# Optimization experiments

Measured on AMD Instinct MI355X. Metric: run time of the kernel, lower is better.

Reference implementation:

```python
import jax, jax.numpy as jnp
import numpy as np

PAD_VALUE = 0.0


def setup_inputs() -> dict:
    key = jax.random.key(0)
    k1, k2 = jax.random.split(key)
    B, DIM, T = 16, 384, 512
    x = jax.random.normal(k1, (B, DIM, T), dtype=jnp.float32)
    duration = jax.random.randint(k2, (B, T), 0, 8, dtype=jnp.int32)
    return {"x": x, "duration": duration, "d_max": T * 8}


def reference(x, duration, d_max):
    """Length regulator (FastSpeech-style).

    x:        (B, dim, T) float32
    duration: (B, T) int32, frames per input timestep
    d_max:    static int, padded output frame length (>= max total duration)

    Returns:
      out:     (B, dim, d_max) expanded/padded tensor
      mel_len: (B,) int32 true output lengths
    """
    B, dim, T = x.shape
    # Guard against all-zero duration rows (original fills them with 1s).
    row_sum = duration.sum(axis=1)  # (B,)
    duration = jnp.where((row_sum == 0)[:, None], jnp.ones_like(duration), duration)

    cum = jnp.cumsum(duration, axis=1)  # (B, T) exclusive-end offsets
    mel_len = cum[:, -1]  # (B,)

    frames = jnp.arange(d_max, dtype=jnp.int32)  # (d_max,)
    # Source index for each output frame: first t with cum[t] > frame.
    idx = jax.vmap(lambda c: jnp.searchsorted(c, frames, side="right"))(cum)  # (B, d_max)
    idx = jnp.clip(idx, 0, T - 1)

    out = jnp.take_along_axis(x, idx[:, None, :], axis=2)  # (B, dim, d_max)
    valid = frames[None, :] < mel_len[:, None]  # (B, d_max)
    out = jnp.where(valid[:, None, :], out, jnp.asarray(PAD_VALUE, x.dtype))
    return out, mel_len
```

## Files before the change

### kernel.cpp

```cpp
#include <hip/hip_runtime.h>

#define B_SZ   16
#define DIM_SZ 384
#define T_SZ   512
#define DMAX   4096
#define DC     8
#define FC     2048

__global__ __launch_bounds__(64) void lr_scan_kernel(const int* __restrict__ duration,
                                                     int* __restrict__ ws_cum,
                                                     int* __restrict__ ws_mel,
                                                     float* __restrict__ mel_out) {
    const int b = blockIdx.x;
    const int l = threadIdx.x;
    const int4* __restrict__ src = (const int4*)(duration + b * T_SZ);
    const int4 a = src[l * 2];
    const int4 c = src[l * 2 + 1];
    int p[8];
    p[0] = a.x;        p[1] = p[0] + a.y; p[2] = p[1] + a.z; p[3] = p[2] + a.w;
    p[4] = p[3] + c.x; p[5] = p[4] + c.y; p[6] = p[5] + c.z; p[7] = p[6] + c.w;
    int s = p[7];
#pragma unroll
    for (int off = 1; off < 64; off <<= 1) {
        const int v = __shfl_up(s, off);
        if (l >= off) s += v;
    }
    const int excl   = s - p[7];
    const int rowsum = __shfl(s, 63);
    int4 o0, o1;
    if (rowsum == 0) {
        const int t0 = l * 8;
        o0 = make_int4(t0 + 1, t0 + 2, t0 + 3, t0 + 4);
        o1 = make_int4(t0 + 5, t0 + 6, t0 + 7, t0 + 8);
    } else {
        o0 = make_int4(excl + p[0], excl + p[1], excl + p[2], excl + p[3]);
        o1 = make_int4(excl + p[4], excl + p[5], excl + p[6], excl + p[7]);
    }
    int4* __restrict__ dst = (int4*)(ws_cum + b * T_SZ);
    dst[l * 2]     = o0;
    dst[l * 2 + 1] = o1;
    if (l == 63) {
        const int ml = (rowsum == 0) ? T_SZ : rowsum;
        ws_mel[b] = ml;
        mel_out[b] = (float)ml;
    }
}

__global__ __launch_bounds__(256) void lr_gather_kernel(const float* __restrict__ x,
                                                        const int* __restrict__ ws_cum,
                                                        const int* __restrict__ ws_mel,
                                                        float* __restrict__ out) {
    __shared__ float s_x[DC * T_SZ];
    __shared__ int   s_cum[T_SZ];
    const int tid = threadIdx.x;
    const int b   = blockIdx.y;
    const int d0  = blockIdx.z * DC;
    const int f0  = blockIdx.x * FC;

    s_cum[tid]       = ws_cum[b * T_SZ + tid];
    s_cum[tid + 256] = ws_cum[b * T_SZ + tid + 256];

    const float4* __restrict__ xsrc = (const float4*)(x + ((size_t)b * DIM_SZ + d0) * T_SZ);
    float4* s_x4 = (float4*)s_x;
#pragma unroll
    for (int i = 0; i < (DC * T_SZ / 4) / 256; ++i)
        s_x4[i * 256 + tid] = xsrc[i * 256 + tid];
    __syncthreads();

    const int mel = ws_mel[b];
    float4* __restrict__ outp = (float4*)(out + (size_t)b * DIM_SZ * DMAX);

#pragma unroll
    for (int g = 0; g < FC / 1024; ++g) {
        const int f  = f0 + g * 1024 + tid * 4;
        const int f4 = f >> 2;
        if (f >= mel) {
            const float4 z = make_float4(0.f, 0.f, 0.f, 0.f);
#pragma unroll
            for (int dd = 0; dd < DC; ++dd)
                outp[(size_t)(d0 + dd) * (DMAX / 4) + f4] = z;
        } else {
            int  idx[4];
            bool valid[4];
#pragma unroll
            for (int j = 0; j < 4; ++j) {
                const int ff = f + j;
                int pos = 0;
#pragma unroll
                for (int step = 256; step > 0; step >>= 1) {
                    if (s_cum[pos + step - 1] <= ff) pos += step;
                }
                idx[j]   = pos;
                valid[j] = (ff < mel);
            }
#pragma unroll
            for (int dd = 0; dd < DC; ++dd) {
                const float* __restrict__ xr = s_x + dd * T_SZ;
                float4 v;
                v.x = valid[0] ? xr[idx[0]] : 0.0f;
                v.y = valid[1] ? xr[idx[1]] : 0.0f;
                v.z = valid[2] ? xr[idx[2]] : 0.0f;
                v.w = valid[3] ? xr[idx[3]] : 0.0f;
                outp[(size_t)(d0 + dd) * (DMAX / 4) + f4] = v;
            }
        }
    }
}

extern "C" void kernel_launch(void* const* d_in, const int* in_sizes, int n_in,
                              void* d_out, int out_size, void* d_ws, size_t ws_size,
                              hipStream_t stream) {
    const float* x        = (const float*)d_in[0];
    const int*   duration = (const int*)d_in[1];

    float* out     = (float*)d_out;
    float* mel_out = out + (size_t)B_SZ * DIM_SZ * DMAX;

    int* ws_cum = (int*)d_ws;
    int* ws_mel = ws_cum + B_SZ * T_SZ;

    lr_scan_kernel<<<B_SZ, 64, 0, stream>>>(duration, ws_cum, ws_mel, mel_out);

    dim3 grid(DMAX / FC, B_SZ, DIM_SZ / DC);
    lr_gather_kernel<<<grid, 256, 0, stream>>>(x, ws_cum, ws_mel, out);
}
```

Before: 116.4 us.

## Precompute per-frame source indices in scan kernel instead of per-block binary search

Result: no change. 118.1 us (+1.4%).

```diff
diff --git a/kernel.cpp b/kernel.cpp
--- a/kernel.cpp
+++ b/kernel.cpp
@@ -8,7 +8,7 @@
 #define FC     2048
 
 __global__ __launch_bounds__(64) void lr_scan_kernel(const int* __restrict__ duration,
-                                                     int* __restrict__ ws_cum,
+                                                     unsigned short* __restrict__ ws_idx,
                                                      int* __restrict__ ws_mel,
                                                      float* __restrict__ mel_out) {
     const int b = blockIdx.x;
@@ -27,38 +27,51 @@
     }
     const int excl   = s - p[7];
     const int rowsum = __shfl(s, 63);
-    int4 o0, o1;
+    unsigned short* __restrict__ idxb = ws_idx + b * DMAX;
     if (rowsum == 0) {
         const int t0 = l * 8;
-        o0 = make_int4(t0 + 1, t0 + 2, t0 + 3, t0 + 4);
-        o1 = make_int4(t0 + 5, t0 + 6, t0 + 7, t0 + 8);
+        ushort4* dst = (ushort4*)(idxb + t0);
+        dst[0] = make_ushort4((unsigned short)(t0 + 0), (unsigned short)(t0 + 1),
+                              (unsigned short)(t0 + 2), (unsigned short)(t0 + 3));
+        dst[1] = make_ushort4((unsigned short)(t0 + 4), (unsigned short)(t0 + 5),
+                              (unsigned short)(t0 + 6), (unsigned short)(t0 + 7));
+        if (l == 63) { ws_mel[b] = T_SZ; mel_out[b] = (float)T_SZ; }
     } else {
-        o0 = make_int4(excl + p[0], excl + p[1], excl + p[2], excl + p[3]);
-        o1 = make_int4(excl + p[4], excl + p[5], excl + p[6], excl + p[7]);
-    }
-    int4* __restrict__ dst = (int4*)(ws_cum + b * T_SZ);
-    dst[l * 2]     = o0;
-    dst[l * 2 + 1] = o1;
-    if (l == 63) {
-        const int ml = (rowsum == 0) ? T_SZ : rowsum;
-        ws_mel[b] = ml;
-        mel_out[b] = (float)ml;
+        int start = excl;
+#pragma unroll
+        for (int k = 0; k < 8; ++k) {
+            const unsigned short t = (unsigned short)(l * 8 + k);
+            const int e = excl + p[k];
+            for (int f = start; f < e; ++f) idxb[f] = t;
+            start = e;
+        }
+        if (l == 63) { ws_mel[b] = rowsum; mel_out[b] = (float)rowsum; }
     }
 }
 
 __global__ __launch_bounds__(256) void lr_gather_kernel(const float* __restrict__ x,
-                                                        const int* __restrict__ ws_cum,
+                                                        const unsigned short* __restrict__ ws_idx,
                                                         const int* __restrict__ ws_mel,
                                                         float* __restrict__ out) {
     __shared__ float s_x[DC * T_SZ];
-    __shared__ int   s_cum[T_SZ];
     const int tid = threadIdx.x;
     const int b   = blockIdx.y;
     const int d0  = blockIdx.z * DC;
     const int f0  = blockIdx.x * FC;
+    const int mel = ws_mel[b];
+    float4* __restrict__ outp = (float4*)(out + (size_t)b * DIM_SZ * DMAX);
 
-    s_cum[tid]       = ws_cum[b * T_SZ + tid];
-    s_cum[tid + 256] = ws_cum[b * T_SZ + tid + 256];
+    if (f0 >= mel) {
+        const float4 z = make_float4(0.f, 0.f, 0.f, 0.f);
+#pragma unroll
+        for (int g = 0; g < FC / 1024; ++g) {
+            const int f4 = ((f0 + g * 1024) >> 2) + tid;
+#pragma unroll
+            for (int dd = 0; dd < DC; ++dd)
+                outp[(size_t)(d0 + dd) * (DMAX / 4) + f4] = z;
+        }
+        return;
+    }
 
     const float4* __restrict__ xsrc = (const float4*)(x + ((size_t)b * DIM_SZ + d0) * T_SZ);
     float4* s_x4 = (float4*)s_x;
@@ -67,8 +80,7 @@
         s_x4[i * 256 + tid] = xsrc[i * 256 + tid];
     __syncthreads();
 
-    const int mel = ws_mel[b];
-    float4* __restrict__ outp = (float4*)(out + (size_t)b * DIM_SZ * DMAX);
+    const ushort4* __restrict__ idxp = (const ushort4*)(ws_idx + (size_t)b * DMAX);
 
 #pragma unroll
     for (int g = 0; g < FC / 1024; ++g) {
@@ -80,19 +92,12 @@
             for (int dd = 0; dd < DC; ++dd)
                 outp[(size_t)(d0 + dd) * (DMAX / 4) + f4] = z;
         } else {
-            int  idx[4];
+            const ushort4 i4 = idxp[f4];
+            int idx[4] = { i4.x & (T_SZ - 1), i4.y & (T_SZ - 1),
+                           i4.z & (T_SZ - 1), i4.w & (T_SZ - 1) };
             bool valid[4];
 #pragma unroll
-            for (int j = 0; j < 4; ++j) {
-                const int ff = f + j;
-                int pos = 0;
-#pragma unroll
-                for (int step = 256; step > 0; step >>= 1) {
-                    if (s_cum[pos + step - 1] <= ff) pos += step;
-                }
-                idx[j]   = pos;
-                valid[j] = (ff < mel);
-            }
+            for (int j = 0; j < 4; ++j) valid[j] = (f + j < mel);
 #pragma unroll
             for (int dd = 0; dd < DC; ++dd) {
                 const float* __restrict__ xr = s_x + dd * T_SZ;
@@ -116,11 +121,11 @@
     float* out     = (float*)d_out;
     float* mel_out = out + (size_t)B_SZ * DIM_SZ * DMAX;
 
-    int* ws_cum = (int*)d_ws;
-    int* ws_mel = ws_cum + B_SZ * T_SZ;
+    unsigned short* ws_idx = (unsigned short*)d_ws;
+    int* ws_mel = (int*)((char*)d_ws + (size_t)B_SZ * DMAX * sizeof(unsigned short));
 
-    lr_scan_kernel<<<B_SZ, 64, 0, stream>>>(duration, ws_cum, ws_mel, mel_out);
+    lr_scan_kernel<<<B_SZ, 64, 0, stream>>>(duration, ws_idx, ws_mel, mel_out);
 
     dim3 grid(DMAX / FC, B_SZ, DIM_SZ / DC);
-    lr_gather_kernel<<<grid, 256, 0, stream>>>(x, ws_cum, ws_mel, out);
+    lr_gather_kernel<<<grid, 256, 0, stream>>>(x, ws_idx, ws_mel, out);
 }
```
